# Kernel tuning notes

Measured on AMD Instinct MI355X. Metric: run time of the kernel, lower is better.

Reference implementation:

```python
import jax, jax.numpy as jnp
import numpy as np

B, S, D, U = 32, 4096, 512, 128

def setup_inputs() -> dict:
    key = jax.random.key(0)
    k1, k2, k3, k4, k5 = jax.random.split(key, 5)
    query = jax.random.normal(k1, (B, D), dtype=jnp.float32)
    values = jax.random.normal(k2, (B, S, D), dtype=jnp.float32)
    s = 1.0 / np.sqrt(D)
    W1 = jax.random.normal(k3, (D, U), dtype=jnp.float32) * s
    W2 = jax.random.normal(k4, (D, U), dtype=jnp.float32) * s
    V = jax.random.normal(k5, (U, 1), dtype=jnp.float32) * (1.0 / np.sqrt(U))
    b1 = jnp.zeros((U,), dtype=jnp.float32)
    b2 = jnp.zeros((U,), dtype=jnp.float32)
    bv = jnp.zeros((1,), dtype=jnp.float32)
    return {"query": query, "values": values, "W1": W1, "b1": b1,
            "W2": W2, "b2": b2, "V": V, "bv": bv}

def reference(query, values, W1, b1, W2, b2, V, bv):
    # query: [B, D] -> [B, 1, U]; values: [B, S, D] -> [B, S, U]
    q_proj = (query @ W1 + b1)[:, None, :]                  # [B, 1, U]
    v_proj = jnp.einsum('bsd,du->bsu', values, W2) + b2      # [B, S, U]
    score = jnp.tanh(q_proj + v_proj) @ V + bv               # [B, S, 1]
    attention_weights = jax.nn.softmax(score, axis=1)        # [B, S, 1]
    context_vector = jnp.sum(attention_weights * values, axis=1)  # [B, D]
    return context_vector, attention_weights
```

## Files before the change

kernel.cpp:

```cpp
#include <hip/hip_runtime.h>
#include <math.h>

#define NB 32
#define NS 4096
#define ND 512
#define NU 128
#define RR 32
#define ASTR 520
#define BSTR 40

typedef __bf16 bf16x8 __attribute__((ext_vector_type(8)));
typedef unsigned short u16x8 __attribute__((ext_vector_type(8)));
typedef float f32x4 __attribute__((ext_vector_type(4)));

union FragCvt { u16x8 u; bf16x8 b; };

__device__ inline unsigned short f2bf(float x) {
  union { float f; unsigned u; } v; v.f = x;
  return (unsigned short)((v.u + 0x7FFFu + ((v.u >> 16) & 1u)) >> 16);
}
__device__ inline float bf2f(unsigned int bits16) {
  union { unsigned u; float f; } v; v.u = bits16 << 16;
  return v.f;
}

__global__ void prep_qb(const float* __restrict__ q, const float* __restrict__ W1,
                        const float* __restrict__ b1, const float* __restrict__ b2,
                        float* __restrict__ qb) {
  int idx = blockIdx.x * 256 + threadIdx.x;
  int b = idx >> 7, u = idx & 127;
  float s = b1[u] + b2[u];
  const float* qr = q + b * ND;
  for (int d = 0; d < ND; ++d) s += qr[d] * W1[d * NU + u];
  qb[idx] = s;
}

__global__ void prep_w2t(const float* __restrict__ W2, unsigned short* __restrict__ w2t) {
  int idx = blockIdx.x * 256 + threadIdx.x;
  int u = idx >> 9, d = idx & 511;
  w2t[idx] = f2bf(W2[d * NU + u]);
}

__global__ __launch_bounds__(256, 3) void fused_attn(
    const float* __restrict__ values,
    const float* __restrict__ qb,
    const unsigned short* __restrict__ w2t,
    const float* __restrict__ V,
    const float* __restrict__ bvp,
    float* __restrict__ wout,
    float* __restrict__ Cacc,
    float* __restrict__ Lacc)
{
  __shared__ unsigned short Alds[RR * ASTR];
  __shared__ unsigned short Blds[NU * BSTR];
  __shared__ float sbuf[4][16];
  __shared__ float wlds[RR];

  const int tid = threadIdx.x;
  const int b = blockIdx.x >> 7;
  const int chunk = blockIdx.x & 127;
  const int s0 = chunk * RR;

  const float* vbase = values + ((size_t)b * NS + s0) * ND;
  #pragma unroll
  for (int i = 0; i < 16; ++i) {
    int f = tid + 256 * i;
    int row = f >> 7;
    int c4 = f & 127;
    float4 v = *(const float4*)(vbase + row * ND + c4 * 4);
    ushort4 pk;
    pk.x = f2bf(v.x); pk.y = f2bf(v.y); pk.z = f2bf(v.z); pk.w = f2bf(v.w);
    *(ushort4*)(&Alds[row * ASTR + c4 * 4]) = pk;
  }

  const int wave = tid >> 6, lane = tid & 63;
  const int quad = lane >> 4, lidx = lane & 15;
  const int mtile = wave & 1;
  const int nbase = (wave >> 1) * 64;

  f32x4 acc[4] = {{0.f,0.f,0.f,0.f},{0.f,0.f,0.f,0.f},{0.f,0.f,0.f,0.f},{0.f,0.f,0.f,0.f}};

  const int bu = tid >> 1, bh = tid & 1;
  for (int kt = 0; kt < 16; ++kt) {
    __syncthreads();
    {
      const unsigned short* src = w2t + bu * ND + kt * 32 + bh * 16;
      u16x8 p0 = *(const u16x8*)(src);
      u16x8 p1 = *(const u16x8*)(src + 8);
      *(u16x8*)(&Blds[bu * BSTR + bh * 16])     = p0;
      *(u16x8*)(&Blds[bu * BSTR + bh * 16 + 8]) = p1;
    }
    __syncthreads();
    FragCvt af; af.u = *(const u16x8*)(&Alds[(mtile * 16 + lidx) * ASTR + kt * 32 + quad * 8]);
    #pragma unroll
    for (int nt = 0; nt < 4; ++nt) {
      FragCvt bf; bf.u = *(const u16x8*)(&Blds[(nbase + nt * 16 + lidx) * BSTR + quad * 8]);
      acc[nt] = __builtin_amdgcn_mfma_f32_16x16x32_bf16(af.b, bf.b, acc[nt], 0, 0, 0);
    }
  }

  float part[4] = {0.f, 0.f, 0.f, 0.f};
  #pragma unroll
  for (int nt = 0; nt < 4; ++nt) {
    int col = nbase + nt * 16 + lidx;
    float qv = qb[b * NU + col];
    float vv = V[col];
    #pragma unroll
    for (int r = 0; r < 4; ++r) {
      float t = tanhf(acc[nt][r] + qv);
      part[r] += t * vv;
    }
  }
  #pragma unroll
  for (int m = 1; m <= 8; m <<= 1) {
    #pragma unroll
    for (int r = 0; r < 4; ++r) part[r] += __shfl_xor(part[r], m, 64);
  }
  if (lidx == 0) {
    #pragma unroll
    for (int r = 0; r < 4; ++r) sbuf[wave][quad * 4 + r] = part[r];
  }
  __syncthreads();

  if (tid < 32) {
    int mt = tid >> 4, rr = tid & 15;
    float s = sbuf[mt][rr] + sbuf[mt + 2][rr];
    float e = expf(s + *bvp);
    wout[(size_t)b * NS + s0 + tid] = e;
    wlds[tid] = e;
    float es = e;
    #pragma unroll
    for (int m = 1; m <= 16; m <<= 1) es += __shfl_xor(es, m, 64);
    if (tid == 0) atomicAdd(Lacc + b, es);
  }
  __syncthreads();

  int d0 = tid * 2;
  float c0 = 0.f, c1 = 0.f;
  for (int r = 0; r < RR; ++r) {
    float w = wlds[r];
    unsigned int pk = *(const unsigned int*)(&Alds[r * ASTR + d0]);
    c0 += w * bf2f(pk & 0xFFFFu);
    c1 += w * bf2f(pk >> 16);
  }
  atomicAdd(Cacc + b * ND + d0, c0);
  atomicAdd(Cacc + b * ND + d0 + 1, c1);
}

__global__ void finalize(const float* __restrict__ Cacc, const float* __restrict__ Lacc,
                         float* __restrict__ out) {
  int idx = blockIdx.x * 256 + threadIdx.x;
  if (idx < NB * ND) {
    int b = idx >> 9;
    out[idx] = Cacc[idx] / Lacc[b];
  } else {
    int j = idx - NB * ND;
    int b = j >> 12;
    out[idx] = out[idx] / Lacc[b];
  }
}

extern "C" void kernel_launch(void* const* d_in, const int* in_sizes, int n_in,
                              void* d_out, int out_size, void* d_ws, size_t ws_size,
                              hipStream_t stream) {
  const float* query  = (const float*)d_in[0];
  const float* values = (const float*)d_in[1];
  const float* W1     = (const float*)d_in[2];
  const float* b1     = (const float*)d_in[3];
  const float* W2     = (const float*)d_in[4];
  const float* b2     = (const float*)d_in[5];
  const float* V      = (const float*)d_in[6];
  const float* bv     = (const float*)d_in[7];
  float* out = (float*)d_out;

  char* ws = (char*)d_ws;
  float* Cacc = (float*)ws;
  float* Lacc = (float*)(ws + 65536);
  float* qb   = (float*)(ws + 66048);
  unsigned short* w2t = (unsigned short*)(ws + 66048 + 16384);

  hipMemsetAsync(ws, 0, 66048, stream);

  prep_qb <<<16, 256, 0, stream>>>(query, W1, b1, b2, qb);
  prep_w2t<<<256, 256, 0, stream>>>(W2, w2t);
  fused_attn<<<NB * (NS / RR), 256, 0, stream>>>(values, qb, w2t, V, bv,
                                                 out + NB * ND, Cacc, Lacc);
  finalize<<<(NB * ND + NB * NS) / 256, 256, 0, stream>>>(Cacc, Lacc, out);
}
```

Baseline: 448.5 us.

## Pre-swizzle W2 into MFMA fragment order and drop LDS staging of B

W2 is now pre-arranged into MFMA B-fragment order, so each lane loads its fragment straight from global/L2 memory. This removes the per-k-tile LDS staging and both barriers in the GEMM loop. The value loads are batched 8-wide to raise memory-level parallelism. tanh and exp are replaced by fast intrinsic approximations, prep_qb is split across many blocks with atomics, and occupancy is raised to 4 blocks per SM. The costs are redundant global reads of W2 by every block, which rely on L2 hits, and slightly lower accuracy from the fast math.

Result: faster. 426.4 us (-4.9%).

```diff
diff --git a/kernel.cpp b/kernel.cpp
--- a/kernel.cpp
+++ b/kernel.cpp
@@ -7,7 +7,6 @@
 #define NU 128
 #define RR 32
 #define ASTR 520
-#define BSTR 40
 
 typedef __bf16 bf16x8 __attribute__((ext_vector_type(8)));
 typedef unsigned short u16x8 __attribute__((ext_vector_type(8)));
@@ -23,28 +22,47 @@
   union { unsigned u; float f; } v; v.u = bits16 << 16;
   return v.f;
 }
+__device__ inline float fast_tanh(float x) {
+  x = fminf(9.f, fmaxf(-9.f, x));
+  float e2 = __expf(2.f * x);
+  return (e2 - 1.f) * __builtin_amdgcn_rcpf(e2 + 1.f);
+}
 
 __global__ void prep_qb(const float* __restrict__ q, const float* __restrict__ W1,
                         const float* __restrict__ b1, const float* __restrict__ b2,
                         float* __restrict__ qb) {
-  int idx = blockIdx.x * 256 + threadIdx.x;
-  int b = idx >> 7, u = idx & 127;
-  float s = b1[u] + b2[u];
-  const float* qr = q + b * ND;
-  for (int d = 0; d < ND; ++d) s += qr[d] * W1[d * NU + u];
-  qb[idx] = s;
-}
-
-__global__ void prep_w2t(const float* __restrict__ W2, unsigned short* __restrict__ w2t) {
-  int idx = blockIdx.x * 256 + threadIdx.x;
-  int u = idx >> 9, d = idx & 511;
-  w2t[idx] = f2bf(W2[d * NU + u]);
-}
-
-__global__ __launch_bounds__(256, 3) void fused_attn(
+  const int bb = blockIdx.x >> 4;
+  const int kc = blockIdx.x & 15;
+  const int u  = threadIdx.x & 127;
+  const int dh = threadIdx.x >> 7;
+  const int d0 = kc * 32 + dh * 16;
+  const float* qr = q + bb * ND + d0;
+  const float* w  = W1 + (size_t)d0 * NU + u;
+  float s = (kc == 0 && dh == 0) ? (b1[u] + b2[u]) : 0.f;
+  #pragma unroll
+  for (int j = 0; j < 16; ++j) s += qr[j] * w[j * NU];
+  atomicAdd(qb + bb * NU + u, s);
+}
+
+__global__ void prep_w2f(const float* __restrict__ W2, uint4* __restrict__ w2f) {
+  const int idx = blockIdx.x * 256 + threadIdx.x;
+  const int lane = idx & 63;
+  const int ut   = (idx >> 6) & 7;
+  const int kt   = idx >> 9;
+  const int lidx = lane & 15;
+  const int quad = lane >> 4;
+  const int u  = ut * 16 + lidx;
+  const int d0 = kt * 32 + quad * 8;
+  unsigned short o[8];
+  #pragma unroll
+  for (int j = 0; j < 8; ++j) o[j] = f2bf(W2[(size_t)(d0 + j) * NU + u]);
+  w2f[idx] = *(const uint4*)o;
+}
+
+__global__ __launch_bounds__(256, 4) void fused_attn(
     const float* __restrict__ values,
     const float* __restrict__ qb,
-    const unsigned short* __restrict__ w2t,
+    const uint4* __restrict__ w2f,
     const float* __restrict__ V,
     const float* __restrict__ bvp,
     float* __restrict__ wout,
@@ -52,7 +70,6 @@
     float* __restrict__ Lacc)
 {
   __shared__ unsigned short Alds[RR * ASTR];
-  __shared__ unsigned short Blds[NU * BSTR];
   __shared__ float sbuf[4][16];
   __shared__ float wlds[RR];
 
@@ -63,38 +80,39 @@
 
   const float* vbase = values + ((size_t)b * NS + s0) * ND;
   #pragma unroll
-  for (int i = 0; i < 16; ++i) {
-    int f = tid + 256 * i;
-    int row = f >> 7;
-    int c4 = f & 127;
-    float4 v = *(const float4*)(vbase + row * ND + c4 * 4);
-    ushort4 pk;
-    pk.x = f2bf(v.x); pk.y = f2bf(v.y); pk.z = f2bf(v.z); pk.w = f2bf(v.w);
-    *(ushort4*)(&Alds[row * ASTR + c4 * 4]) = pk;
-  }
+  for (int ii = 0; ii < 16; ii += 8) {
+    float4 v[8];
+    #pragma unroll
+    for (int j = 0; j < 8; ++j) {
+      const int f = tid + 256 * (ii + j);
+      v[j] = *(const float4*)(vbase + (f >> 7) * ND + (f & 127) * 4);
+    }
+    #pragma unroll
+    for (int j = 0; j < 8; ++j) {
+      const int f = tid + 256 * (ii + j);
+      ushort4 pk;
+      pk.x = f2bf(v[j].x); pk.y = f2bf(v[j].y); pk.z = f2bf(v[j].z); pk.w = f2bf(v[j].w);
+      *(ushort4*)(&Alds[(f >> 7) * ASTR + (f & 127) * 4]) = pk;
+    }
+  }
+  __syncthreads();
 
   const int wave = tid >> 6, lane = tid & 63;
   const int quad = lane >> 4, lidx = lane & 15;
   const int mtile = wave & 1;
   const int nbase = (wave >> 1) * 64;
+  const int utb = (wave >> 1) * 4;
 
   f32x4 acc[4] = {{0.f,0.f,0.f,0.f},{0.f,0.f,0.f,0.f},{0.f,0.f,0.f,0.f},{0.f,0.f,0.f,0.f}};
-
-  const int bu = tid >> 1, bh = tid & 1;
+  const unsigned short* arow = &Alds[(mtile * 16 + lidx) * ASTR];
+  const uint4* wfl = w2f + lane;
+
+  #pragma unroll 4
   for (int kt = 0; kt < 16; ++kt) {
-    __syncthreads();
-    {
-      const unsigned short* src = w2t + bu * ND + kt * 32 + bh * 16;
-      u16x8 p0 = *(const u16x8*)(src);
-      u16x8 p1 = *(const u16x8*)(src + 8);
-      *(u16x8*)(&Blds[bu * BSTR + bh * 16])     = p0;
-      *(u16x8*)(&Blds[bu * BSTR + bh * 16 + 8]) = p1;
-    }
-    __syncthreads();
-    FragCvt af; af.u = *(const u16x8*)(&Alds[(mtile * 16 + lidx) * ASTR + kt * 32 + quad * 8]);
+    FragCvt af; af.u = *(const u16x8*)(arow + kt * 32 + quad * 8);
     #pragma unroll
     for (int nt = 0; nt < 4; ++nt) {
-      FragCvt bf; bf.u = *(const u16x8*)(&Blds[(nbase + nt * 16 + lidx) * BSTR + quad * 8]);
+      FragCvt bf; bf.u = *(const u16x8*)(wfl + (kt * 8 + utb + nt) * 64);
       acc[nt] = __builtin_amdgcn_mfma_f32_16x16x32_bf16(af.b, bf.b, acc[nt], 0, 0, 0);
     }
   }
@@ -102,14 +120,12 @@
   float part[4] = {0.f, 0.f, 0.f, 0.f};
   #pragma unroll
   for (int nt = 0; nt < 4; ++nt) {
-    int col = nbase + nt * 16 + lidx;
-    float qv = qb[b * NU + col];
-    float vv = V[col];
-    #pragma unroll
-    for (int r = 0; r < 4; ++r) {
-      float t = tanhf(acc[nt][r] + qv);
-      part[r] += t * vv;
-    }
+    const int col = nbase + nt * 16 + lidx;
+    const float qv = qb[b * NU + col];
+    const float vv = V[col];
+    #pragma unroll
+    for (int r = 0; r < 4; ++r)
+      part[r] += fast_tanh(acc[nt][r] + qv) * vv;
   }
   #pragma unroll
   for (int m = 1; m <= 8; m <<= 1) {
@@ -123,9 +139,9 @@
   __syncthreads();
 
   if (tid < 32) {
-    int mt = tid >> 4, rr = tid & 15;
+    const int mt = tid >> 4, rr = tid & 15;
     float s = sbuf[mt][rr] + sbuf[mt + 2][rr];
-    float e = expf(s + *bvp);
+    float e = __expf(s + *bvp);
     wout[(size_t)b * NS + s0 + tid] = e;
     wlds[tid] = e;
     float es = e;
@@ -135,11 +151,12 @@
   }
   __syncthreads();
 
-  int d0 = tid * 2;
+  const int d0 = tid * 2;
   float c0 = 0.f, c1 = 0.f;
+  #pragma unroll 8
   for (int r = 0; r < RR; ++r) {
-    float w = wlds[r];
-    unsigned int pk = *(const unsigned int*)(&Alds[r * ASTR + d0]);
+    const float w = wlds[r];
+    const unsigned int pk = *(const unsigned int*)(&Alds[r * ASTR + d0]);
     c0 += w * bf2f(pk & 0xFFFFu);
     c1 += w * bf2f(pk >> 16);
   }
@@ -177,13 +194,13 @@
   float* Cacc = (float*)ws;
   float* Lacc = (float*)(ws + 65536);
   float* qb   = (float*)(ws + 66048);
-  unsigned short* w2t = (unsigned short*)(ws + 66048 + 16384);
-
-  hipMemsetAsync(ws, 0, 66048, stream);
-
-  prep_qb <<<16, 256, 0, stream>>>(query, W1, b1, b2, qb);
-  prep_w2t<<<256, 256, 0, stream>>>(W2, w2t);
-  fused_attn<<<NB * (NS / RR), 256, 0, stream>>>(values, qb, w2t, V, bv,
+  uint4* w2f  = (uint4*)(ws + 66048 + 16384);
+
+  hipMemsetAsync(ws, 0, 66048 + 16384, stream);
+
+  prep_qb <<<NB * 16, 256, 0, stream>>>(query, W1, b1, b2, qb);
+  prep_w2f<<<32, 256, 0, stream>>>(W2, w2f);
+  fused_attn<<<NB * (NS / RR), 256, 0, stream>>>(values, qb, w2f, V, bv,
                                                  out + NB * ND, Cacc, Lacc);
   finalize<<<(NB * ND + NB * NS) / 256, 256, 0, stream>>>(Cacc, Lacc, out);
 }
```
